# Kernel tuning notes

Hardware: AMD Instinct MI355X
Metric: run time of the kernel (lower is better)

The kernel has to match this reference:

```python
import jax, jax.numpy as jnp
import numpy as np

# Llama-7B FFN up-proj quantized with HQQ 4-bit, group_size=64, axis=0
OUT, IN, GS = 11008, 4096, 64
G = OUT * IN // GS  # 704512 groups


def setup_inputs() -> dict:
    key = jax.random.key(0)
    k1, k2, k3, k4, k5 = jax.random.split(key, 5)
    # packed 4-bit weights: two nibbles per byte, shape [GS//2, G]
    W_q = jax.random.randint(k1, (GS // 2, G), 0, 256, dtype=jnp.int32)
    # per-group scale (meta['scale'] = 1/scale from quantize) and zero
    scale = jax.random.uniform(k2, (1, G), jnp.float32, minval=1e-3, maxval=1e-2)
    zero = jax.random.uniform(k3, (1, G), jnp.float32, minval=0.0, maxval=15.0)
    # decode-style activations: 8 sequences, 1 token each
    x = jax.random.normal(k4, (8, 1, IN), dtype=jnp.float32)
    bias = jax.random.normal(k5, (OUT,), dtype=jnp.float32) * 0.01
    return {"W_q": W_q, "scale": scale, "zero": zero, "x": x, "bias": bias}


def reference(W_q, scale, zero, x, bias):
    # BitPack.unpack_4bit_u8: high nibble rows stacked on low nibble rows
    hi = (W_q >> 4) & 0xF
    lo = W_q & 0xF
    W_q_p = jnp.concatenate([hi, lo], axis=0).astype(x.dtype)  # [GS, G]
    # Quantizer.dequantize: (W_q_p - zero) * scale, reshape to weight shape
    W_r = ((W_q_p - zero) * scale).reshape(OUT, IN)  # [out, in]
    # torch.nn.functional.linear(x, W_r, bias)
    return jnp.einsum('bsi,oi->bso', x, W_r) + bias
```

## Files before the change

### kernel.cpp

```cpp
#include <hip/hip_runtime.h>


#define OUT_ 11008
#define IN_ 4096
#define G_ 704512
#define OC_ 172

__global__ void zero_out_kernel(float* __restrict__ out) {
    const int t = blockIdx.x * 256 + threadIdx.x;
    if (t < 8 * OUT_) out[t] = 0.f;
}

__global__ __launch_bounds__(256, 4)
void hqq_gemv(const int* __restrict__ Wq, const float* __restrict__ scale,
              const float* __restrict__ zero, const float* __restrict__ x,
              const float* __restrict__ bias, float* __restrict__ out) {
    const int lane = threadIdx.x;
    const int ty   = threadIdx.y;
    const int oc   = blockIdx.y;
    const int ks   = blockIdx.z;
    const int rq0  = blockIdx.x * 8 + ty * 2;

    const int kbase = ks * (IN_ / 2);
    const long gb = (long)oc * IN_ + kbase;
    const int* __restrict__ wqA = Wq + (long)rq0 * G_ + gb;
    const int* __restrict__ wqB = wqA + G_;
    const float* __restrict__ sp = scale + gb;
    const float* __restrict__ zp = zero + gb;
    const float* __restrict__ xp = x + kbase;

    float acc[4][8];
#pragma unroll
    for (int r = 0; r < 4; ++r)
#pragma unroll
        for (int b = 0; b < 8; ++b) acc[r][b] = 0.f;

    int i = lane * 4;
    int4 qa = *(const int4*)(wqA + i);
    int4 qb = *(const int4*)(wqB + i);

#pragma unroll
    for (int it = 0; it < 8; ++it) {
        const float4 s4 = *(const float4*)(sp + i);
        const float4 z4 = *(const float4*)(zp + i);
        int4 qa_n, qb_n;
        if (it < 7) {
            qa_n = *(const int4*)(wqA + i + 256);
            qb_n = *(const int4*)(wqB + i + 256);
        }
        const float ss[4] = {s4.x, s4.y, s4.z, s4.w};
        const float zs[4] = {-z4.x * s4.x, -z4.y * s4.y, -z4.z * s4.z, -z4.w * s4.w};
        const int qsA[4] = {qa.x, qa.y, qa.z, qa.w};
        const int qsB[4] = {qb.x, qb.y, qb.z, qb.w};

        float w[4][4];
#pragma unroll
        for (int j = 0; j < 4; ++j) {
            w[0][j] = fmaf((float)((qsA[j] >> 4) & 0xF), ss[j], zs[j]);
            w[1][j] = fmaf((float)( qsA[j]       & 0xF), ss[j], zs[j]);
            w[2][j] = fmaf((float)((qsB[j] >> 4) & 0xF), ss[j], zs[j]);
            w[3][j] = fmaf((float)( qsB[j]       & 0xF), ss[j], zs[j]);
        }
#pragma unroll
        for (int b = 0; b < 8; ++b) {
            const float4 xb = *(const float4*)(xp + b * IN_ + i);
#pragma unroll
            for (int r = 0; r < 4; ++r) {
                float a = acc[r][b];
                a = fmaf(xb.x, w[r][0], a);
                a = fmaf(xb.y, w[r][1], a);
                a = fmaf(xb.z, w[r][2], a);
                a = fmaf(xb.w, w[r][3], a);
                acc[r][b] = a;
            }
        }
        if (it < 7) { qa = qa_n; qb = qb_n; }
        i += 256;
    }

#pragma unroll
    for (int r = 0; r < 4; ++r)
#pragma unroll
        for (int b = 0; b < 8; ++b) {
            float v = acc[r][b];
#pragma unroll
            for (int off = 32; off > 0; off >>= 1)
                v += __shfl_down(v, off, 64);
            acc[r][b] = v;
        }

    if (lane == 0) {
        const int o[4] = {rq0 * OC_ + oc, (rq0 + 32) * OC_ + oc,
                          (rq0 + 1) * OC_ + oc, (rq0 + 33) * OC_ + oc};
#pragma unroll
        for (int r = 0; r < 4; ++r) {
            const float bb = (ks == 0) ? bias[o[r]] : 0.f;
#pragma unroll
            for (int b = 0; b < 8; ++b)
                atomicAdd(out + b * OUT_ + o[r], acc[r][b] + bb);
        }
    }
}

extern "C" void kernel_launch(void* const* d_in, const int* in_sizes, int n_in,
                              void* d_out, int out_size, void* d_ws, size_t ws_size,
                              hipStream_t stream) {
    const int*   Wq    = (const int*)d_in[0];
    const float* scale = (const float*)d_in[1];
    const float* zero  = (const float*)d_in[2];
    const float* x     = (const float*)d_in[3];
    const float* bias  = (const float*)d_in[4];
    float* out = (float*)d_out;

    zero_out_kernel<<<(8 * OUT_ + 255) / 256, 256, 0, stream>>>(out);

    dim3 grid(4, OC_, 2);
    dim3 block(64, 4);
    hqq_gemv<<<grid, block, 0, stream>>>(Wq, scale, zero, x, bias, out);
}
```

Measured before the change: 177.4 us.

## Stage scale/zero/x in LDS, prefetch all weights, replace atomics with workspace reduce

Each block copies its scale, zero and activation slices into shared memory and issues all packed-weight loads up front before computing. The atomic accumulation and zero-fill kernel are replaced by plain partial-sum stores to a workspace and a separate reduce kernel that adds bias. This is meant to cut redundant global reads, raise memory-level parallelism and avoid atomics. In exchange it uses large LDS and many registers, lowering occupancy, and adds an extra kernel launch.

```diff
diff --git a/kernel.cpp b/kernel.cpp
--- a/kernel.cpp
+++ b/kernel.cpp
@@ -5,29 +5,52 @@
 #define IN_ 4096
 #define G_ 704512
 #define OC_ 172
+#define KS 2
+#define KC (IN_ / KS)
+#define ITERS (KC / 256)
 
-__global__ void zero_out_kernel(float* __restrict__ out) {
-    const int t = blockIdx.x * 256 + threadIdx.x;
-    if (t < 8 * OUT_) out[t] = 0.f;
-}
-
-__global__ __launch_bounds__(256, 4)
+__global__ __launch_bounds__(256, 2)
 void hqq_gemv(const int* __restrict__ Wq, const float* __restrict__ scale,
               const float* __restrict__ zero, const float* __restrict__ x,
-              const float* __restrict__ bias, float* __restrict__ out) {
+              float* __restrict__ ws) {
+    __shared__ float s_lds[KC];
+    __shared__ float z_lds[KC];
+    __shared__ float x_lds[8 * KC];
+
     const int lane = threadIdx.x;
     const int ty   = threadIdx.y;
+    const int tid  = ty * 64 + lane;
     const int oc   = blockIdx.y;
     const int ks   = blockIdx.z;
     const int rq0  = blockIdx.x * 8 + ty * 2;
 
-    const int kbase = ks * (IN_ / 2);
+    const int kbase = ks * KC;
     const long gb = (long)oc * IN_ + kbase;
+
+#pragma unroll
+    for (int r = 0; r < KC / 1024; ++r) {
+        const int off = r * 1024 + tid * 4;
+        *(float4*)(s_lds + off) = *(const float4*)(scale + gb + off);
+        *(float4*)(z_lds + off) = *(const float4*)(zero + gb + off);
+    }
+#pragma unroll
+    for (int r = 0; r < 8 * KC / 1024; ++r) {
+        const int off = r * 1024 + tid * 4;
+        const int b = off >> 11;
+        const int k = off & (KC - 1);
+        *(float4*)(x_lds + off) = *(const float4*)(x + b * IN_ + kbase + k);
+    }
+
     const int* __restrict__ wqA = Wq + (long)rq0 * G_ + gb;
     const int* __restrict__ wqB = wqA + G_;
-    const float* __restrict__ sp = scale + gb;
-    const float* __restrict__ zp = zero + gb;
-    const float* __restrict__ xp = x + kbase;
+    int4 qA[ITERS], qB[ITERS];
+#pragma unroll
+    for (int it = 0; it < ITERS; ++it) {
+        qA[it] = *(const int4*)(wqA + it * 256 + lane * 4);
+        qB[it] = *(const int4*)(wqB + it * 256 + lane * 4);
+    }
+
+    __syncthreads();
 
     float acc[4][8];
 #pragma unroll
@@ -35,23 +58,15 @@
 #pragma unroll
         for (int b = 0; b < 8; ++b) acc[r][b] = 0.f;
 
-    int i = lane * 4;
-    int4 qa = *(const int4*)(wqA + i);
-    int4 qb = *(const int4*)(wqB + i);
-
 #pragma unroll
-    for (int it = 0; it < 8; ++it) {
-        const float4 s4 = *(const float4*)(sp + i);
-        const float4 z4 = *(const float4*)(zp + i);
-        int4 qa_n, qb_n;
-        if (it < 7) {
-            qa_n = *(const int4*)(wqA + i + 256);
-            qb_n = *(const int4*)(wqB + i + 256);
-        }
+    for (int it = 0; it < ITERS; ++it) {
+        const int i = it * 256 + lane * 4;
+        const float4 s4 = *(const float4*)(s_lds + i);
+        const float4 z4 = *(const float4*)(z_lds + i);
         const float ss[4] = {s4.x, s4.y, s4.z, s4.w};
         const float zs[4] = {-z4.x * s4.x, -z4.y * s4.y, -z4.z * s4.z, -z4.w * s4.w};
-        const int qsA[4] = {qa.x, qa.y, qa.z, qa.w};
-        const int qsB[4] = {qb.x, qb.y, qb.z, qb.w};
+        const int qsA[4] = {qA[it].x, qA[it].y, qA[it].z, qA[it].w};
+        const int qsB[4] = {qB[it].x, qB[it].y, qB[it].z, qB[it].w};
 
         float w[4][4];
 #pragma unroll
@@ -63,7 +78,7 @@
         }
 #pragma unroll
         for (int b = 0; b < 8; ++b) {
-            const float4 xb = *(const float4*)(xp + b * IN_ + i);
+            const float4 xb = *(const float4*)(x_lds + b * KC + i);
 #pragma unroll
             for (int r = 0; r < 4; ++r) {
                 float a = acc[r][b];
@@ -74,8 +89,6 @@
                 acc[r][b] = a;
             }
         }
-        if (it < 7) { qa = qa_n; qb = qb_n; }
-        i += 256;
     }
 
 #pragma unroll
@@ -92,14 +105,25 @@
     if (lane == 0) {
         const int o[4] = {rq0 * OC_ + oc, (rq0 + 32) * OC_ + oc,
                           (rq0 + 1) * OC_ + oc, (rq0 + 33) * OC_ + oc};
+        float* __restrict__ wp = ws + (long)ks * 8 * OUT_;
 #pragma unroll
-        for (int r = 0; r < 4; ++r) {
-            const float bb = (ks == 0) ? bias[o[r]] : 0.f;
+        for (int r = 0; r < 4; ++r)
 #pragma unroll
             for (int b = 0; b < 8; ++b)
-                atomicAdd(out + b * OUT_ + o[r], acc[r][b] + bb);
-        }
+                wp[b * OUT_ + o[r]] = acc[r][b];
     }
+}
+
+__global__ void hqq_reduce(const float* __restrict__ ws,
+                           const float* __restrict__ bias,
+                           float* __restrict__ out) {
+    const int t = blockIdx.x * 256 + threadIdx.x;
+    if (t >= 8 * OUT_) return;
+    const int o = t % OUT_;
+    float v = bias[o];
+#pragma unroll
+    for (int k = 0; k < KS; ++k) v += ws[k * 8 * OUT_ + t];
+    out[t] = v;
 }
 
 extern "C" void kernel_launch(void* const* d_in, const int* in_sizes, int n_in,
@@ -111,10 +135,10 @@
     const float* x     = (const float*)d_in[3];
     const float* bias  = (const float*)d_in[4];
     float* out = (float*)d_out;
+    float* ws  = (float*)d_ws;
 
-    zero_out_kernel<<<(8 * OUT_ + 255) / 256, 256, 0, stream>>>(out);
-
-    dim3 grid(4, OC_, 2);
+    dim3 grid(4, OC_, KS);
     dim3 block(64, 4);
-    hqq_gemv<<<grid, block, 0, stream>>>(Wq, scale, zero, x, bias, out);
+    hqq_gemv<<<grid, block, 0, stream>>>(Wq, scale, zero, x, ws);
+    hqq_reduce<<<(8 * OUT_ + 255) / 256, 256, 0, stream>>>(ws, bias, out);
 }
```

Measured after the change: 152.2 us. 1.17x faster.
